# Kernel optimization log

Hardware: AMD Instinct MI355X
Metric: run time of the kernel (lower is better)

Reference implementation:

```python
import jax, jax.numpy as jnp
import numpy as np

# Faithful JAX translation of fastmax_function with mask=True, p=1, normalize=0.
# In that branch the torch code sets temperature = 1 and uses a0 = a1 = 1.

def setup_inputs() -> dict:
    key = jax.random.key(0)
    kq, kk, kv = jax.random.split(key, 3)
    b, h, n, d = 2, 8, 8192, 32
    q = jax.random.normal(kq, (b, h, n, d), dtype=jnp.float32)
    k = jax.random.normal(kk, (b, h, n, d), dtype=jnp.float32)
    v = jax.random.normal(kv, (b, h, n, d), dtype=jnp.float32)
    return {"q": q, "k": k, "v": v}


def reference(q, k, v):
    # q, k, v: (b, h, n, d); causal (mask=True), p=1, a0=a1=1, temperature=1
    b, h, n, d = q.shape
    # first term: running sum of values
    first = jnp.cumsum(v, axis=2)                                  # (b,h,n,d)
    # second term: q_i . (sum_{j<=i} k_j v_j^T)
    kv = jnp.einsum('bhnd,bhne->bhnde', k, v)                      # (b,h,n,d,d)
    kv_cs = jnp.cumsum(kv, axis=2)                                 # (b,h,n,d,d)
    second = jnp.einsum('bhnd,bhnde->bhne', q, kv_cs)              # (b,h,n,d)
    # denominator: i + q_i . (sum_{j<=i} k_j)
    k_cs = jnp.cumsum(k, axis=2)                                   # (b,h,n,d)
    div1 = jnp.arange(1, n + 1, dtype=q.dtype)                     # (n,)
    div2 = jnp.einsum('bhnd,bhnd->bhn', q, k_cs)                   # (b,h,n)
    div = (div1[None, None, :] + div2)[..., None]                  # (b,h,n,1)
    return (first + second) / div
```

## Files before the change

kernel.cpp:

```cpp
#include <hip/hip_runtime.h>


#define D      32
#define C      64
#define NCHUNK 128
#define GSIZE  8
#define NGROUP 16
#define BH     16
#define NBLK   (BH * NCHUNK)
#define STATE  1088
#define STCH   1152

typedef __attribute__((ext_vector_type(8))) short bf16x8;
typedef __attribute__((ext_vector_type(4))) float f32x4;
typedef __attribute__((ext_vector_type(4))) unsigned short u16x4;

__device__ __forceinline__ unsigned short f2bf(float x) {
  union { float f; unsigned u; } c; c.f = x;
  unsigned r = (c.u + 0x7FFFu + ((c.u >> 16) & 1u)) >> 16;
  return (unsigned short)r;
}
__device__ __forceinline__ float bf2f(unsigned short u) {
  union { unsigned u; float f; } c; c.u = ((unsigned)u) << 16;
  return c.f;
}
__device__ __forceinline__ int permcol(int e) {
  return (e & 1) ? (16 + (e >> 1)) : (e >> 1);
}
__device__ __forceinline__ float4 add4(float4 a, float4 b) {
  return make_float4(a.x + b.x, a.y + b.y, a.z + b.z, a.w + b.w);
}

__global__ __launch_bounds__(256) void state_scan_kernel(
    const float* __restrict__ k, const float* __restrict__ v,
    unsigned short* __restrict__ states, float* __restrict__ totals) {
  int blk = blockIdx.x;
  int c0  = blk * GSIZE;
  const float4* kp = (const float4*)k + (size_t)c0 * 512;
  const float4* vp = (const float4*)v + (size_t)c0 * 512;

  __shared__ __align__(16) unsigned short kT[D * 72];
  __shared__ __align__(16) unsigned short vT[D * 72];
  __shared__ __align__(16) float4 psK[256];
  __shared__ __align__(16) float4 psV[256];

  int t  = threadIdx.x;
  int j0 = t >> 3;
  int cb = (t & 7) * 4;
  int lane = t & 63, w = t >> 6;
  int m16 = lane & 15, quad = lane >> 4;
  int mb = w >> 1, nb = w & 1;
  int d1b = 16 * mb + quad * 4;
  int d2  = 16 * nb + m16;
  int n   = permcol(d2);

  float pref[4] = {0.f, 0.f, 0.f, 0.f};
  float tailpref = 0.f;

  float4 kA = kp[t], kB = kp[t + 256];
  float4 vA = vp[t], vB = vp[t + 256];

  for (int ci = 0; ci < GSIZE; ++ci) {
    {
      const float* ka = &kA.x; const float* kb = &kB.x;
      const float* va = &vA.x; const float* vb = &vB.x;
#pragma unroll
      for (int cc = 0; cc < 4; ++cc) {
        kT[(cb + cc) * 72 + j0]      = f2bf(ka[cc]);
        kT[(cb + cc) * 72 + j0 + 32] = f2bf(kb[cc]);
        vT[(cb + cc) * 72 + j0]      = f2bf(va[cc]);
        vT[(cb + cc) * 72 + j0 + 32] = f2bf(vb[cc]);
      }
      psK[t] = make_float4(kA.x + kB.x, kA.y + kB.y, kA.z + kB.z, kA.w + kB.w);
      psV[t] = make_float4(vA.x + vB.x, vA.y + vB.y, vA.z + vB.z, vA.w + vB.w);
    }
    __syncthreads();

    if (ci + 1 < GSIZE) {
      const float4* kn = kp + (size_t)(ci + 1) * 512;
      const float4* vn = vp + (size_t)(ci + 1) * 512;
      kA = kn[t]; kB = kn[t + 256];
      vA = vn[t]; vB = vn[t + 256];
    }

    f32x4 acc = {0.f, 0.f, 0.f, 0.f};
#pragma unroll
    for (int kb2 = 0; kb2 < 2; ++kb2) {
      bf16x8 a = *(const bf16x8*)&kT[(16 * mb + m16) * 72 + kb2 * 32 + quad * 8];
      bf16x8 b = *(const bf16x8*)&vT[(16 * nb + m16) * 72 + kb2 * 32 + quad * 8];
      acc = __builtin_amdgcn_mfma_f32_16x16x32_bf16(a, b, acc, 0, 0, 0);
    }
    float csum = 0.f;
    if (t < 64) {
      int ee = t & 31;
      const float* ps = (t < 32) ? (const float*)psK : (const float*)psV;
#pragma unroll
      for (int m = 0; m < 32; ++m) csum += ps[ee + 32 * m];
    }

    unsigned short* stC = states + (size_t)(c0 + ci) * STCH;
    *(u16x4*)&stC[n * 32 + d1b] =
        (u16x4){f2bf(pref[0]), f2bf(pref[1]), f2bf(pref[2]), f2bf(pref[3])};
#pragma unroll
    for (int reg = 0; reg < 4; ++reg) pref[reg] += acc[reg];
    if (t < 64) {
      ((float*)(stC + 1024))[t] = tailpref;
      tailpref += csum;
    }
    __syncthreads();
  }

  float* tp = totals + (size_t)blk * STATE;
  *(float4*)&tp[n * 32 + d1b] =
      make_float4(pref[0], pref[1], pref[2], pref[3]);
  if (t < 64) tp[1024 + t] = tailpref;
}

__global__ __launch_bounds__(256) void totals_scan_kernel(float* __restrict__ totals) {
  int gidx = blockIdx.x * 256 + threadIdx.x;
  int bh = gidx / STATE;
  int e  = gidx % STATE;
  float* base = totals + (size_t)(bh * NGROUP) * STATE + e;
  float a = 0.f;
#pragma unroll
  for (int g = 0; g < NGROUP; ++g) {
    float s = base[(size_t)g * STATE];
    base[(size_t)g * STATE] = a;
    a += s;
  }
}

__global__ __launch_bounds__(256) void output_kernel(
    const float* __restrict__ q, const float* __restrict__ k,
    const float* __restrict__ v, const unsigned short* __restrict__ states,
    const float* __restrict__ totals, float* __restrict__ out) {
  int blk = blockIdx.x;
  int c   = blk & 127;
  int bh  = blk >> 7;
  int g   = c >> 3;
  size_t off = (size_t)blk * (C * D);
  const float4* qp4 = (const float4*)q + (size_t)blk * 512;
  const float4* kp4 = (const float4*)k + (size_t)blk * 512;
  const float4* vp4 = (const float4*)v + (size_t)blk * 512;
  const unsigned short* stc = states + (size_t)blk * STCH;
  const float* tb = totals + (size_t)(bh * NGROUP + g) * STATE;

  __shared__ __align__(16) unsigned short qbf[C * 40];
  __shared__ __align__(16) unsigned short kbf[C * 40];
  __shared__ __align__(16) unsigned short vTbf[D * 72];
  __shared__ __align__(16) unsigned short kvTbf[D * 40];
  __shared__ __align__(16) unsigned short Tbf[C * 72];
  __shared__ __align__(16) float q_s[C * 36];
  __shared__ __align__(16) float kc_s[C * 36];
  __shared__ __align__(16) float gtot[8 * 32];
  __shared__ __align__(16) float kpre_s[D], vpre_s[D], invdiv_s[C];

  int t  = threadIdx.x;
  int j0 = t >> 3;
  int cb = (t & 7) * 4;

  float4 qA = qp4[t], qB = qp4[t + 256];
  float4 kA = kp4[t], kB = kp4[t + 256];
  float4 vA = vp4[t], vB = vp4[t + 256];
  uint2  su  = *(const uint2*)&stc[t * 4];
  float4 tv4 = *(const float4*)&tb[t * 4];
  float4 tail = make_float4(0.f, 0.f, 0.f, 0.f);
  if (t < 16)
    tail = add4(*(const float4*)((const float*)(stc + 1024) + 4 * t),
                *(const float4*)&tb[1024 + 4 * t]);

  for (int z = t; z < (C * 72) / 8; z += 256)
    ((uint4*)Tbf)[z] = make_uint4(0, 0, 0, 0);

  *(float4*)&q_s[j0 * 36 + cb]         = qA;
  *(float4*)&q_s[(j0 + 32) * 36 + cb]  = qB;
  *(float4*)&kc_s[j0 * 36 + cb]        = kA;
  *(float4*)&kc_s[(j0 + 32) * 36 + cb] = kB;
  *(u16x4*)&qbf[j0 * 40 + cb] =
      (u16x4){f2bf(qA.x), f2bf(qA.y), f2bf(qA.z), f2bf(qA.w)};
  *(u16x4*)&qbf[(j0 + 32) * 40 + cb] =
      (u16x4){f2bf(qB.x), f2bf(qB.y), f2bf(qB.z), f2bf(qB.w)};
  *(u16x4*)&kbf[j0 * 40 + cb] =
      (u16x4){f2bf(kA.x), f2bf(kA.y), f2bf(kA.z), f2bf(kA.w)};
  *(u16x4*)&kbf[(j0 + 32) * 40 + cb] =
      (u16x4){f2bf(kB.x), f2bf(kB.y), f2bf(kB.z), f2bf(kB.w)};
  {
    const float* va = &vA.x; const float* vb = &vB.x;
#pragma unroll
    for (int cc = 0; cc < 4; ++cc) {
      int n = permcol(cb + cc);
      vTbf[n * 72 + j0]      = f2bf(va[cc]);
      vTbf[n * 72 + j0 + 32] = f2bf(vb[cc]);
    }
  }
  {
    float s0 = bf2f((unsigned short)(su.x & 0xffff)) + tv4.x;
    float s1 = bf2f((unsigned short)(su.x >> 16))    + tv4.y;
    float s2 = bf2f((unsigned short)(su.y & 0xffff)) + tv4.z;
    float s3 = bf2f((unsigned short)(su.y >> 16))    + tv4.w;
    *(u16x4*)&kvTbf[(t >> 3) * 40 + (t & 7) * 4] =
        (u16x4){f2bf(s0), f2bf(s1), f2bf(s2), f2bf(s3)};
  }
  if (t < 8)            ((float4*)kpre_s)[t]     = tail;
  else if (t < 16)      ((float4*)vpre_s)[t - 8] = tail;
  __syncthreads();

  int lane = t & 63, w = t >> 6;
  int m16 = lane & 15, quad = lane >> 4;

  const bf16x8 aQ = *(const bf16x8*)&qbf[(16 * w + m16) * 40 + quad * 8];
  for (int jb = 0; jb <= w; ++jb) {
    bf16x8 bK = *(const bf16x8*)&kbf[(16 * jb + m16) * 40 + quad * 8];
    f32x4 cS = {0.f, 0.f, 0.f, 0.f};
    cS = __builtin_amdgcn_mfma_f32_16x16x32_bf16(aQ, bK, cS, 0, 0, 0);
    int jcol = 16 * jb + m16;
#pragma unroll
    for (int reg = 0; reg < 4; ++reg) {
      int i = 16 * w + quad * 4 + reg;
      float tv = (jcol <= i) ? (1.f + cS[reg]) : 0.f;
      Tbf[i * 72 + jcol] = f2bf(tv);
    }
  }
  int rg = t >> 5;
  int e  = t & 31;
  float vals[8];
  {
    float run = 0.f;
#pragma unroll
    for (int r = 0; r < 8; ++r) {
      vals[r] = kc_s[(rg * 8 + r) * 36 + e];
      run += vals[r];
    }
    gtot[rg * 32 + e] = run;
  }
  __syncthreads();

  {
    float offv = kpre_s[e];
    for (int g2 = 0; g2 < rg; ++g2) offv += gtot[g2 * 32 + e];
    float cacc = offv;
#pragma unroll
    for (int r = 0; r < 8; ++r) {
      cacc += vals[r];
      kc_s[(rg * 8 + r) * 36 + e] = cacc;
    }
  }
  __syncthreads();

  if (t < 64) {
    int i = t;
    float dp = 0.f;
#pragma unroll
    for (int d4 = 0; d4 < 8; ++d4) {
      float4 qv = *(const float4*)&q_s[i * 36 + 4 * d4];
      float4 kc = *(const float4*)&kc_s[i * 36 + 4 * d4];
      dp += qv.x * kc.x + qv.y * kc.y + qv.z * kc.z + qv.w * kc.w;
    }
    invdiv_s[i] = 1.f / ((float)(c * C + i + 1) + dp);
  }
  f32x4 o0 = {0.f, 0.f, 0.f, 0.f}, o1 = {0.f, 0.f, 0.f, 0.f};
  {
    bf16x8 b0 = *(const bf16x8*)&kvTbf[(m16)      * 40 + quad * 8];
    bf16x8 b1 = *(const bf16x8*)&kvTbf[(16 + m16) * 40 + quad * 8];
    o0 = __builtin_amdgcn_mfma_f32_16x16x32_bf16(aQ, b0, o0, 0, 0, 0);
    o1 = __builtin_amdgcn_mfma_f32_16x16x32_bf16(aQ, b1, o1, 0, 0, 0);
  }
  int kbcnt = (w >= 2) ? 2 : 1;
  for (int kb2 = 0; kb2 < kbcnt; ++kb2) {
    bf16x8 aT = *(const bf16x8*)&Tbf[(16 * w + m16) * 72 + kb2 * 32 + quad * 8];
    bf16x8 b0 = *(const bf16x8*)&vTbf[(m16)      * 72 + kb2 * 32 + quad * 8];
    bf16x8 b1 = *(const bf16x8*)&vTbf[(16 + m16) * 72 + kb2 * 32 + quad * 8];
    o0 = __builtin_amdgcn_mfma_f32_16x16x32_bf16(aT, b0, o0, 0, 0, 0);
    o1 = __builtin_amdgcn_mfma_f32_16x16x32_bf16(aT, b1, o1, 0, 0, 0);
  }
  __syncthreads();

  int e0 = 2 * m16;
#pragma unroll
  for (int reg = 0; reg < 4; ++reg) {
    int i = 16 * w + quad * 4 + reg;
    float id = invdiv_s[i];
    float2 o;
    o.x = (vpre_s[e0]     + o0[reg]) * id;
    o.y = (vpre_s[e0 + 1] + o1[reg]) * id;
    *(float2*)&out[off + (size_t)i * D + e0] = o;
  }
}

extern "C" void kernel_launch(void* const* d_in, const int* in_sizes, int n_in,
                              void* d_out, int out_size, void* d_ws, size_t ws_size,
                              hipStream_t stream) {
  const float* q = (const float*)d_in[0];
  const float* k = (const float*)d_in[1];
  const float* v = (const float*)d_in[2];
  float* out = (float*)d_out;
  unsigned short* states = (unsigned short*)d_ws;
  float* totals = (float*)(states + (size_t)NBLK * STCH);

  state_scan_kernel<<<BH * NGROUP, 256, 0, stream>>>(k, v, states, totals);
  totals_scan_kernel<<<(BH * STATE) / 256, 256, 0, stream>>>(totals);
  output_kernel<<<NBLK, 256, 0, stream>>>(q, k, v, states, totals, out);
}
```

Measured before the change: 104.3 us.

## Halve scan group size, fold totals scan into output kernel, alias LDS buffers

```diff
diff --git a/kernel.cpp b/kernel.cpp
--- a/kernel.cpp
+++ b/kernel.cpp
@@ -4,8 +4,8 @@
 #define D      32
 #define C      64
 #define NCHUNK 128
-#define GSIZE  8
-#define NGROUP 16
+#define GSIZE  4
+#define NGROUP 32
 #define BH     16
 #define NBLK   (BH * NCHUNK)
 #define STATE  1088
@@ -116,41 +116,28 @@
   if (t < 64) tp[1024 + t] = tailpref;
 }
 
-__global__ __launch_bounds__(256) void totals_scan_kernel(float* __restrict__ totals) {
-  int gidx = blockIdx.x * 256 + threadIdx.x;
-  int bh = gidx / STATE;
-  int e  = gidx % STATE;
-  float* base = totals + (size_t)(bh * NGROUP) * STATE + e;
-  float a = 0.f;
-#pragma unroll
-  for (int g = 0; g < NGROUP; ++g) {
-    float s = base[(size_t)g * STATE];
-    base[(size_t)g * STATE] = a;
-    a += s;
-  }
-}
-
-__global__ __launch_bounds__(256) void output_kernel(
+__global__ __launch_bounds__(256, 4) void output_kernel(
     const float* __restrict__ q, const float* __restrict__ k,
     const float* __restrict__ v, const unsigned short* __restrict__ states,
     const float* __restrict__ totals, float* __restrict__ out) {
   int blk = blockIdx.x;
   int c   = blk & 127;
   int bh  = blk >> 7;
-  int g   = c >> 3;
+  int g   = c >> 2;
   size_t off = (size_t)blk * (C * D);
   const float4* qp4 = (const float4*)q + (size_t)blk * 512;
   const float4* kp4 = (const float4*)k + (size_t)blk * 512;
   const float4* vp4 = (const float4*)v + (size_t)blk * 512;
   const unsigned short* stc = states + (size_t)blk * STCH;
-  const float* tb = totals + (size_t)(bh * NGROUP + g) * STATE;
-
-  __shared__ __align__(16) unsigned short qbf[C * 40];
-  __shared__ __align__(16) unsigned short kbf[C * 40];
+  const float* tb0 = totals + (size_t)(bh * NGROUP) * STATE;
+
+  __shared__ __align__(16) char uA[10240];
+  unsigned short* qbf = (unsigned short*)uA;
+  unsigned short* kbf = (unsigned short*)(uA + 5120);
+  float* q_s = (float*)uA;
   __shared__ __align__(16) unsigned short vTbf[D * 72];
   __shared__ __align__(16) unsigned short kvTbf[D * 40];
   __shared__ __align__(16) unsigned short Tbf[C * 72];
-  __shared__ __align__(16) float q_s[C * 36];
   __shared__ __align__(16) float kc_s[C * 36];
   __shared__ __align__(16) float gtot[8 * 32];
   __shared__ __align__(16) float kpre_s[D], vpre_s[D], invdiv_s[C];
@@ -163,17 +150,19 @@
   float4 kA = kp4[t], kB = kp4[t + 256];
   float4 vA = vp4[t], vB = vp4[t + 256];
   uint2  su  = *(const uint2*)&stc[t * 4];
-  float4 tv4 = *(const float4*)&tb[t * 4];
+  float4 tv4 = make_float4(0.f, 0.f, 0.f, 0.f);
+  for (int g2 = 0; g2 < g; ++g2)
+    tv4 = add4(tv4, *(const float4*)&tb0[(size_t)g2 * STATE + 4 * t]);
   float4 tail = make_float4(0.f, 0.f, 0.f, 0.f);
-  if (t < 16)
-    tail = add4(*(const float4*)((const float*)(stc + 1024) + 4 * t),
-                *(const float4*)&tb[1024 + 4 * t]);
+  if (t < 16) {
+    tail = *(const float4*)((const float*)(stc + 1024) + 4 * t);
+    for (int g2 = 0; g2 < g; ++g2)
+      tail = add4(tail, *(const float4*)&tb0[(size_t)g2 * STATE + 1024 + 4 * t]);
+  }
 
   for (int z = t; z < (C * 72) / 8; z += 256)
     ((uint4*)Tbf)[z] = make_uint4(0, 0, 0, 0);
 
-  *(float4*)&q_s[j0 * 36 + cb]         = qA;
-  *(float4*)&q_s[(j0 + 32) * 36 + cb]  = qB;
   *(float4*)&kc_s[j0 * 36 + cb]        = kA;
   *(float4*)&kc_s[(j0 + 32) * 36 + cb] = kB;
   *(u16x4*)&qbf[j0 * 40 + cb] =
@@ -245,6 +234,8 @@
       kc_s[(rg * 8 + r) * 36 + e] = cacc;
     }
   }
+  *(float4*)&q_s[j0 * 36 + cb]        = qA;
+  *(float4*)&q_s[(j0 + 32) * 36 + cb] = qB;
   __syncthreads();
 
   if (t < 64) {
@@ -298,6 +289,5 @@
   float* totals = (float*)(states + (size_t)NBLK * STCH);
 
   state_scan_kernel<<<BH * NGROUP, 256, 0, stream>>>(k, v, states, totals);
-  totals_scan_kernel<<<(BH * STATE) / 256, 256, 0, stream>>>(totals);
   output_kernel<<<NBLK, 256, 0, stream>>>(q, k, v, states, totals, out);
 }
```

Result: slower. 119.7 us (+14.7%).
